# Kernel tuning notes

Hardware: AMD Instinct MI355X
Metric: run time of the kernel (lower is better)

## Reference

```python
import jax, jax.numpy as jnp
import numpy as np

N = 100000   # num_nodes
E = 1600000  # num_edges
R = 8        # num_rels
B = 4        # num_bases
D = 64       # inp_dim = h_dim = out_dim


def setup_inputs() -> dict:
    key = jax.random.key(0)
    ks = jax.random.split(key, 16)
    s = 1.0 / np.sqrt(D)
    inp = {
        'h': jax.random.normal(ks[0], (N, D), jnp.float32),
        'src': jax.random.randint(ks[1], (E,), 0, N),
        'dst': jax.random.randint(ks[2], (E,), 0, N),
        'etype': jax.random.randint(ks[3], (E,), 0, R),
        'norm': jax.random.uniform(ks[4], (E, 1), jnp.float32),
    }
    for i in range(3):  # i2h, hidden, h2o layers (basis decomposition)
        inp[f'bases{i}'] = jax.random.normal(ks[5 + 2 * i], (B, D, D), jnp.float32) * s
        inp[f'wcomp{i}'] = jax.random.normal(ks[6 + 2 * i], (R, B), jnp.float32) * s
    inp['dec_w1'] = jax.random.normal(ks[11], (D, D), jnp.float32) * s
    inp['dec_b1'] = jnp.zeros((D,), jnp.float32)
    inp['dec_w2'] = jax.random.normal(ks[12], (D, 1), jnp.float32) * s
    inp['dec_b2'] = jnp.zeros((1,), jnp.float32)
    return inp


def rgcn_layer(h, src, dst, etype, norm, bases, wcomp, activate):
    # basis decomposition: W_r = sum_b wcomp[r,b] * bases[b]
    W = jnp.einsum('rb,bio->rio', wcomp, bases)           # [R, D, D]
    # transform all nodes under every relation (dense GEMM), then gather per edge
    Ht = jnp.einsum('ni,rio->rno', h, W).reshape(R * N, -1)  # [R*N, D]
    msg = Ht[etype * N + src] * norm                      # [E, D] gather + norm
    out = jax.ops.segment_sum(msg, dst, num_segments=N)   # scatter-add to dst
    return jax.nn.relu(out) if activate else out


def reference(h, src, dst, etype, norm, bases0, wcomp0, bases1, wcomp1,
              bases2, wcomp2, dec_w1, dec_b1, dec_w2, dec_b2):
    # EncoderRGCN: i2h (relu) -> hidden (relu) -> h2o (no activation)
    h1 = rgcn_layer(h, src, dst, etype, norm, bases0, wcomp0, True)
    h2 = rgcn_layer(h1, src, dst, etype, norm, bases1, wcomp1, True)
    henc = rgcn_layer(h2, src, dst, etype, norm, bases2, wcomp2, False)
    # AttributeDecoder: Linear -> ReLU -> Linear(reconstruct_dim=1)
    d1 = jax.nn.relu(henc @ dec_w1 + dec_b1)
    rec = (d1 @ dec_w2 + dec_b2).squeeze()                # [N]
    return rec, henc
```

## Files before the change

### kernel.cpp

```cpp
#include <hip/hip_runtime.h>

typedef _Float16 half8 __attribute__((ext_vector_type(8)));
typedef _Float16 half4 __attribute__((ext_vector_type(4)));
typedef _Float16 half2v __attribute__((ext_vector_type(2)));
typedef float floatx4 __attribute__((ext_vector_type(4)));

constexpr int NN = 100000;
constexpr int EE = 1600000;
constexpr int NBK = 196;
constexpr int CHUNK = 3125;
constexpr int CAPB = 12288;
constexpr int NDCAP = 48;

__global__ __launch_bounds__(256) void k_part(const int* __restrict__ dst,
                                              const int* __restrict__ src,
                                              const int* __restrict__ etype,
                                              const float* __restrict__ norm,
                                              int* __restrict__ gcur,
                                              int2* __restrict__ part) {
  __shared__ int2 ldata[CHUNK];
  __shared__ unsigned char lbkt[CHUNK];
  __shared__ int lhist[NBK], lbase[NBK + 1], lcur[NBK], gbase[NBK];
  __shared__ int sh[256];
  const int tid = threadIdx.x;
  const int e0 = blockIdx.x * CHUNK;

  for (int b = tid; b < NBK; b += 256) lhist[b] = 0;
  __syncthreads();
  for (int i = tid; i < CHUNK; i += 256)
    atomicAdd(&lhist[dst[e0 + i] >> 9], 1);
  __syncthreads();
  {
    const int v = (tid < NBK) ? lhist[tid] : 0;
    sh[tid] = v;
    __syncthreads();
    int run = v;
    for (int d = 1; d < 256; d <<= 1) {
      int t = (tid >= d) ? sh[tid - d] : 0;
      __syncthreads();
      run += t;
      sh[tid] = run;
      __syncthreads();
    }
    if (tid < NBK) {
      lbase[tid] = run - v;
      lcur[tid] = 0;
      gbase[tid] = tid * CAPB + atomicAdd(&gcur[tid], v);
    }
    if (tid == 0) lbase[NBK] = CHUNK;
  }
  __syncthreads();
  for (int i = tid; i < CHUNK; i += 256) {
    const int e = e0 + i;
    const int d = dst[e], s = src[e], et = etype[e];
    const _Float16 nh = (_Float16)norm[e];
    const unsigned short n16 = __builtin_bit_cast(unsigned short, nh);
    const int bk = d >> 9;
    const int pos = lbase[bk] + atomicAdd(&lcur[bk], 1);
    ldata[pos] = make_int2((d << 15) | (s >> 2), (s & 3) | (et << 2) | ((int)n16 << 5));
    lbkt[pos] = (unsigned char)bk;
  }
  __syncthreads();
  for (int i = tid; i < CHUNK; i += 256) {
    const int bk = (int)lbkt[i];
    part[gbase[bk] + (i - lbase[bk])] = ldata[i];
  }
}

__global__ __launch_bounds__(512) void k_part2(const int* __restrict__ gcur,
                                               const int2* __restrict__ part,
                                               int* __restrict__ off,
                                               int2* __restrict__ em) {
  __shared__ int hcnt[512];
  __shared__ int wred[8];
  __shared__ int swsum[8];
  const int tid = threadIdx.x;
  const int bk = blockIdx.x;
  const int nb0 = bk << 9;
  const int2* __restrict__ pp = part + (size_t)bk * CAPB;

  {
    int pv = (tid < bk) ? gcur[tid] : 0;
    for (int d = 32; d > 0; d >>= 1) pv += __shfl_down(pv, d);
    if ((tid & 63) == 0) wred[tid >> 6] = pv;
  }
  hcnt[tid] = 0;
  __syncthreads();
  int base = 0;
#pragma unroll
  for (int w = 0; w < 8; ++w) base += wred[w];
  const int cntb = gcur[bk];

  for (int i = tid; i < cntb; i += 512)
    atomicAdd(&hcnt[(((unsigned)pp[i].x) >> 15) & 511], 1);
  __syncthreads();
  const int v = hcnt[tid];
  int incl = v;
  for (int d = 1; d < 64; d <<= 1) {
    const int t = __shfl_up(incl, d);
    if ((tid & 63) >= d) incl += t;
  }
  if ((tid & 63) == 63) swsum[tid >> 6] = incl;
  __syncthreads();
  int pre = 0;
  for (int w = 0; w < (tid >> 6); ++w) pre += swsum[w];
  const int excl = pre + incl - v;
  {
    const int n = nb0 + tid;
    if (n < NN) off[n] = base + excl;
  }
  if (bk == NBK - 1 && tid == 0) off[NN] = EE;
  hcnt[tid] = excl;
  __syncthreads();
  for (int i = tid; i < cntb; i += 512) {
    const int2 r = pp[i];
    const int d = ((unsigned)r.x) >> 15;
    const int s = ((r.x & 0x7FFF) << 2) | (r.y & 3);
    const int et = (r.y >> 2) & 7;
    const unsigned short n16 = (unsigned short)((r.y >> 5) & 0xFFFF);
    const float nf = (float)__builtin_bit_cast(_Float16, n16);
    const int pos = atomicAdd(&hcnt[d & 511], 1);
    em[base + pos] = make_int2((et << 20) | s, __float_as_int(nf));
  }
}


__global__ __launch_bounds__(256) void k_prep(const float* __restrict__ h,
                                              _Float16* __restrict__ hh,
                                              const float* __restrict__ b0,
                                              const float* __restrict__ b1,
                                              const float* __restrict__ b2,
                                              _Float16* __restrict__ bbt,
                                              int* __restrict__ gcur) {
  const int bx = blockIdx.x;
  if (bx == 0 && threadIdx.x < NBK) gcur[threadIdx.x] = 0;
  if (bx < 6250) {
    const int i = bx * 256 + threadIdx.x;
    const float4 v = *(const float4*)&h[(size_t)i * 4];
    half4 o = {(_Float16)v.x, (_Float16)v.y, (_Float16)v.z, (_Float16)v.w};
    *(half4*)&hh[(size_t)i * 4] = o;
  } else {
    const int g = (bx - 6250) >> 6;
    const int idx = ((bx - 6250) & 63) * 256 + threadIdx.x;
    const float* bases = (g == 0) ? b0 : (g == 1) ? b1 : b2;
    const int o = idx >> 8, k = idx & 255;
    const int b = k >> 6, i = k & 63;
    bbt[g * 16384 + idx] = (_Float16)bases[b * 4096 + i * 64 + o];
  }
}

__global__ __launch_bounds__(256, 8) void k_layer(const _Float16* __restrict__ hh,
                                                  const int* __restrict__ off,
                                                  const int2* __restrict__ em,
                                                  const float* __restrict__ wcomp,
                                                  const _Float16* __restrict__ bbt,
                                                  _Float16* __restrict__ out16,
                                                  float* __restrict__ out32) {
  __shared__ _Float16 Ash[16 * 264];
  __shared__ int  ems_s[16 * NDCAP];
  __shared__ int2 ems_c[16 * NDCAP];
  __shared__ float4 wcs[8];
  __shared__ int offs[17];
  __shared__ int ovf;
  const int tid = threadIdx.x;
  const int lane = tid & 63;
  const int wv = tid >> 6;
  const int n0 = blockIdx.x * 16;

  if (tid < 17) offs[tid] = off[n0 + tid];
  if (tid == 0) ovf = 0;
  if (tid < 8) wcs[tid] = ((const float4*)wcomp)[tid];
  for (int i = tid; i < 16 * NDCAP; i += 256) {
    ems_s[i] = 0;
    ems_c[i] = make_int2(0, 0);
  }
  __syncthreads();

  const int e0 = offs[0];
  const int len = offs[16] - e0;
  for (int i = tid; i < len; i += 256) {
    const int g = e0 + i;
    const int2 r = em[g];
    int lo = 0, hi = 15;
    while (lo < hi) { const int mid = (lo + hi + 1) >> 1; if (offs[mid] <= g) lo = mid; else hi = mid - 1; }
    const int rank = g - offs[lo];
    const int et = r.x >> 20;
    const int s = r.x & 0xFFFFF;
    const float nf = __int_as_float(r.y);
    const float4 w = wcs[et];
    const _Float16 c0 = (_Float16)(nf * w.x), c1 = (_Float16)(nf * w.y);
    const _Float16 c2 = (_Float16)(nf * w.z), c3 = (_Float16)(nf * w.w);
    const half2v p01 = {c0, c1}, p23 = {c2, c3};
    if (rank < NDCAP) {
      ems_s[lo * NDCAP + rank] = s;
      ems_c[lo * NDCAP + rank] = make_int2(
          __builtin_bit_cast(int, p01), __builtin_bit_cast(int, p23));
    } else ovf = 1;
  }
  __syncthreads();

  if (!ovf) {
    const int fl = lane & 31;
    const int eg = lane >> 5;
    const half2v* __restrict__ hp = (const half2v*)hh;
    for (int q = 0; q < 4; ++q) {
      const int m = wv * 4 + q;
      const int cnt = offs[m + 1] - offs[m];
      const int nbat = (cnt + 15) >> 4;
      const int* sp = &ems_s[m * NDCAP + eg * 8];
      const int2* cp = &ems_c[m * NDCAP + eg * 8];
      half2v a0 = {0, 0}, a1 = {0, 0}, a2 = {0, 0}, a3 = {0, 0};
      for (int b = 0; b < nbat; ++b) {
        int s8[8];
#pragma unroll
        for (int j = 0; j < 8; ++j) s8[j] = sp[b * 16 + j];
        half2v hv[8];
#pragma unroll
        for (int j = 0; j < 8; ++j)
          hv[j] = hp[(unsigned)s8[j] * 32u + fl];
#pragma unroll
        for (int j = 0; j < 8; ++j) {
          const int2 cc = cp[b * 16 + j];
          const half2v c01 = __builtin_bit_cast(half2v, cc.x);
          const half2v c23 = __builtin_bit_cast(half2v, cc.y);
          a0 = a0 + hv[j] * __builtin_shufflevector(c01, c01, 0, 0);
          a1 = a1 + hv[j] * __builtin_shufflevector(c01, c01, 1, 1);
          a2 = a2 + hv[j] * __builtin_shufflevector(c23, c23, 0, 0);
          a3 = a3 + hv[j] * __builtin_shufflevector(c23, c23, 1, 1);
        }
      }
      a0 = a0 + __builtin_bit_cast(half2v, __shfl_xor(__builtin_bit_cast(int, a0), 32));
      a1 = a1 + __builtin_bit_cast(half2v, __shfl_xor(__builtin_bit_cast(int, a1), 32));
      a2 = a2 + __builtin_bit_cast(half2v, __shfl_xor(__builtin_bit_cast(int, a2), 32));
      a3 = a3 + __builtin_bit_cast(half2v, __shfl_xor(__builtin_bit_cast(int, a3), 32));
      if (eg == 0) {
        _Float16* ar = &Ash[m * 264];
        *(half2v*)&ar[0 * 64 + 2 * fl] = a0;
        *(half2v*)&ar[1 * 64 + 2 * fl] = a1;
        *(half2v*)&ar[2 * 64 + 2 * fl] = a2;
        *(half2v*)&ar[3 * 64 + 2 * fl] = a3;
      }
    }
  } else {
    const _Float16* hl = hh + lane;
    for (int q = 0; q < 4; ++q) {
      const int m = wv * 4 + q;
      const int p0 = offs[m], p1 = offs[m + 1];
      float a0 = 0.f, a1 = 0.f, a2 = 0.f, a3 = 0.f;
      for (int p = p0; p < p1; p += 8) {
#pragma unroll
        for (int j = 0; j < 8; ++j) {
          const bool live = (p + j < p1);
          const int idx = live ? p + j : p1 - 1;
          const int2 mm = em[idx];
          const float hv = (float)hl[(size_t)(mm.x & 0xFFFFF) << 6];
          const float wn = live ? __int_as_float(mm.y) : 0.f;
          const float4 w = wcs[mm.x >> 20];
          const float t = wn * hv;
          a0 = fmaf(t, w.x, a0); a1 = fmaf(t, w.y, a1);
          a2 = fmaf(t, w.z, a2); a3 = fmaf(t, w.w, a3);
        }
      }
      _Float16* ar = &Ash[m * 264];
      ar[lane]       = (_Float16)a0;
      ar[64 + lane]  = (_Float16)a1;
      ar[128 + lane] = (_Float16)a2;
      ar[192 + lane] = (_Float16)a3;
    }
  }
  __syncthreads();

  const int col = lane & 15;
  const int quad = lane >> 4;
  const int obase = wv * 16 + col;
  const _Float16* ap = &Ash[col * 264 + quad * 8];
  const _Float16* bp = &bbt[(size_t)obase * 256 + quad * 8];
  floatx4 acc = {0.f, 0.f, 0.f, 0.f};
#pragma unroll
  for (int s = 0; s < 8; ++s) {
    const half8 af = *(const half8*)(ap + s * 32);
    const half8 bf = *(const half8*)(bp + s * 32);
    acc = __builtin_amdgcn_mfma_f32_16x16x32_f16(af, bf, acc, 0, 0, 0);
  }
  if (out16) {
#pragma unroll
    for (int r = 0; r < 4; ++r) {
      const float c = fmaxf(acc[r], 0.f);
      out16[(size_t)(n0 + quad * 4 + r) * 64 + obase] = (_Float16)c;
    }
  } else {
#pragma unroll
    for (int r = 0; r < 4; ++r) {
      out32[(size_t)(n0 + quad * 4 + r) * 64 + obase] = acc[r];
    }
  }
}

__global__ __launch_bounds__(256) void k_dec(const float* __restrict__ henc,
                                             const float* __restrict__ w1,
                                             const float* __restrict__ b1,
                                             const float* __restrict__ w2,
                                             const float* __restrict__ b2,
                                             float* __restrict__ rec) {
  __shared__ float w1s[64 * 64];
  __shared__ float hs[16 * 68];
  const int tid = threadIdx.x;
  for (int r = tid; r < 1024; r += 256)
    *(float4*)&w1s[r * 4] = *(const float4*)&w1[r * 4];
  const int og = tid & 15;
  const int nl = tid >> 4;
  const float4 wv2 = *(const float4*)&w2[og * 4];
  const float4 bv1 = *(const float4*)&b1[og * 4];
  const float b2v = b2[0];
  for (int t0 = blockIdx.x * 16; t0 < NN; t0 += gridDim.x * 16) {
    __syncthreads();
    {
      const float4 hv = *(const float4*)&henc[(size_t)t0 * 64 + tid * 4];
      *(float4*)&hs[(tid >> 4) * 68 + (tid & 15) * 4] = hv;
    }
    __syncthreads();
    float4 acc = bv1;
    const float* hr = &hs[nl * 68];
#pragma unroll 8
    for (int i = 0; i < 64; ++i) {
      const float hv = hr[i];
      const float4 wv = *(const float4*)&w1s[i * 64 + og * 4];
      acc.x = fmaf(hv, wv.x, acc.x); acc.y = fmaf(hv, wv.y, acc.y);
      acc.z = fmaf(hv, wv.z, acc.z); acc.w = fmaf(hv, wv.w, acc.w);
    }
    acc.x = fmaxf(acc.x, 0.f); acc.y = fmaxf(acc.y, 0.f);
    acc.z = fmaxf(acc.z, 0.f); acc.w = fmaxf(acc.w, 0.f);
    float v = acc.x * wv2.x + acc.y * wv2.y + acc.z * wv2.z + acc.w * wv2.w;
    v += __shfl_xor(v, 1); v += __shfl_xor(v, 2);
    v += __shfl_xor(v, 4); v += __shfl_xor(v, 8);
    if (og == 0) rec[t0 + nl] = v + b2v;
  }
}


extern "C" void kernel_launch(void* const* d_in, const int* in_sizes, int n_in,
                              void* d_out, int out_size, void* d_ws, size_t ws_size,
                              hipStream_t stream) {
  const float* h     = (const float*)d_in[0];
  const int*   src   = (const int*)d_in[1];
  const int*   dst   = (const int*)d_in[2];
  const int*   etype = (const int*)d_in[3];
  const float* norm  = (const float*)d_in[4];
  const float* bases[3] = {(const float*)d_in[5], (const float*)d_in[7], (const float*)d_in[9]};
  const float* wcomp[3] = {(const float*)d_in[6], (const float*)d_in[8], (const float*)d_in[10]};
  const float* dw1 = (const float*)d_in[11];
  const float* db1 = (const float*)d_in[12];
  const float* dw2 = (const float*)d_in[13];
  const float* db2 = (const float*)d_in[14];

  float* rec  = (float*)d_out;
  float* henc = (float*)d_out + NN;

  char* ws = (char*)d_ws;
  int*      off    = (int*)(ws + 0);
  int*      gcur   = (int*)(ws + 400512);
  int2*     em     = (int2*)(ws + 402560);
  _Float16* hh     = (_Float16*)(ws + 13202560);
  _Float16* h1f    = (_Float16*)(ws + 26002560);
  _Float16* h2f    = (_Float16*)(ws + 38802560);
  _Float16* bbt    = (_Float16*)(ws + 51602560);
  int2*     part   = (int2*)h1f;

  k_prep<<<6250 + 192, 256, 0, stream>>>(h, hh, bases[0], bases[1], bases[2], bbt, gcur);

  k_part<<<512, 256, 0, stream>>>(dst, src, etype, norm, gcur, part);
  k_part2<<<NBK, 512, 0, stream>>>(gcur, part, off, em);

  k_layer<<<NN / 16, 256, 0, stream>>>(hh,  off, em, wcomp[0], bbt,         h1f, nullptr);
  k_layer<<<NN / 16, 256, 0, stream>>>(h1f, off, em, wcomp[1], bbt + 16384, h2f, nullptr);
  k_layer<<<NN / 16, 256, 0, stream>>>(h2f, off, em, wcomp[2], bbt + 32768, nullptr, henc);

  k_dec<<<256, 256, 0, stream>>>(henc, dw1, db1, dw2, db2, rec);
}
```

Baseline: 347.3 us.

## Encode local dst index in edge records and software-pipeline gather across nodes

Packs the destination node's low four bits into the edge record during partitioning, so the layer kernel no longer binary-searches offsets per edge. Restructures the per-wave gather loop to double-buffer the hh row loads, prefetching the next node's first batch while the current node's FMAs run, and uses int4 vector LDS loads for indices and coefficients. Also vectorises the shared-memory zeroing. This adds register pressure from two eight-entry buffers and sixteen accumulators, which could reduce occupancy.

```diff
diff --git a/kernel.cpp b/kernel.cpp
--- a/kernel.cpp
+++ b/kernel.cpp
@@ -120,7 +120,7 @@
     const unsigned short n16 = (unsigned short)((r.y >> 5) & 0xFFFF);
     const float nf = (float)__builtin_bit_cast(_Float16, n16);
     const int pos = atomicAdd(&hcnt[d & 511], 1);
-    em[base + pos] = make_int2((et << 20) | s, __float_as_int(nf));
+    em[base + pos] = make_int2(((d & 15) << 23) | (et << 20) | s, __float_as_int(nf));
   }
 }
 
@@ -170,9 +170,12 @@
   if (tid < 17) offs[tid] = off[n0 + tid];
   if (tid == 0) ovf = 0;
   if (tid < 8) wcs[tid] = ((const float4*)wcomp)[tid];
-  for (int i = tid; i < 16 * NDCAP; i += 256) {
-    ems_s[i] = 0;
-    ems_c[i] = make_int2(0, 0);
+  {
+    const int4 z4 = make_int4(0, 0, 0, 0);
+    int4* zs = (int4*)ems_s;
+    int4* zc = (int4*)ems_c;
+    if (tid < 192) zs[tid] = z4;
+    for (int i = tid; i < 384; i += 256) zc[i] = z4;
   }
   __syncthreads();
 
@@ -181,10 +184,9 @@
   for (int i = tid; i < len; i += 256) {
     const int g = e0 + i;
     const int2 r = em[g];
-    int lo = 0, hi = 15;
-    while (lo < hi) { const int mid = (lo + hi + 1) >> 1; if (offs[mid] <= g) lo = mid; else hi = mid - 1; }
+    const int lo = (r.x >> 23) & 15;
     const int rank = g - offs[lo];
-    const int et = r.x >> 20;
+    const int et = (r.x >> 20) & 7;
     const int s = r.x & 0xFFFFF;
     const float nf = __int_as_float(r.y);
     const float4 w = wcs[et];
@@ -199,46 +201,91 @@
   }
   __syncthreads();
 
+#define LOADB(mm, bb, hv)                                                      \
+  {                                                                            \
+    const int4* sp4_ = (const int4*)&ems_s[(mm) * NDCAP + (bb) * 16 + eg * 8]; \
+    const int4 sa_ = sp4_[0], sb_ = sp4_[1];                                   \
+    hv[0] = hp[(unsigned)sa_.x * 32u + fl];                                    \
+    hv[1] = hp[(unsigned)sa_.y * 32u + fl];                                    \
+    hv[2] = hp[(unsigned)sa_.z * 32u + fl];                                    \
+    hv[3] = hp[(unsigned)sa_.w * 32u + fl];                                    \
+    hv[4] = hp[(unsigned)sb_.x * 32u + fl];                                    \
+    hv[5] = hp[(unsigned)sb_.y * 32u + fl];                                    \
+    hv[6] = hp[(unsigned)sb_.z * 32u + fl];                                    \
+    hv[7] = hp[(unsigned)sb_.w * 32u + fl];                                    \
+  }
+
+#define FMAQ(mm, bb, hv, aq)                                                   \
+  {                                                                            \
+    const int4* cp4_ = (const int4*)&ems_c[(mm) * NDCAP + (bb) * 16 + eg * 8]; \
+    _Pragma("unroll")                                                          \
+    for (int k_ = 0; k_ < 4; ++k_) {                                           \
+      const int4 c_ = cp4_[k_];                                                \
+      const half2v pa01_ = __builtin_bit_cast(half2v, c_.x);                   \
+      const half2v pa23_ = __builtin_bit_cast(half2v, c_.y);                   \
+      const half2v pb01_ = __builtin_bit_cast(half2v, c_.z);                   \
+      const half2v pb23_ = __builtin_bit_cast(half2v, c_.w);                   \
+      aq[0] = aq[0] + hv[2 * k_] * __builtin_shufflevector(pa01_, pa01_, 0, 0);\
+      aq[1] = aq[1] + hv[2 * k_] * __builtin_shufflevector(pa01_, pa01_, 1, 1);\
+      aq[2] = aq[2] + hv[2 * k_] * __builtin_shufflevector(pa23_, pa23_, 0, 0);\
+      aq[3] = aq[3] + hv[2 * k_] * __builtin_shufflevector(pa23_, pa23_, 1, 1);\
+      aq[0] = aq[0] + hv[2 * k_ + 1] * __builtin_shufflevector(pb01_, pb01_, 0, 0);\
+      aq[1] = aq[1] + hv[2 * k_ + 1] * __builtin_shufflevector(pb01_, pb01_, 1, 1);\
+      aq[2] = aq[2] + hv[2 * k_ + 1] * __builtin_shufflevector(pb23_, pb23_, 0, 0);\
+      aq[3] = aq[3] + hv[2 * k_ + 1] * __builtin_shufflevector(pb23_, pb23_, 1, 1);\
+    }                                                                          \
+  }
+
   if (!ovf) {
     const int fl = lane & 31;
     const int eg = lane >> 5;
     const half2v* __restrict__ hp = (const half2v*)hh;
+    const int mb = wv * 4;
+    const int oA = offs[mb], oB = offs[mb + 1], oC = offs[mb + 2],
+              oD = offs[mb + 3], oE = offs[mb + 4];
+    const int c0n = oB - oA, c1n = oC - oB, c2n = oD - oC, c3n = oE - oD;
+    const int nb0_ = (c0n > 0) ? ((c0n + 15) >> 4) : 1;
+    const int nb1_ = (c1n > 0) ? ((c1n + 15) >> 4) : 1;
+    const int nb2_ = (c2n > 0) ? ((c2n + 15) >> 4) : 1;
+    const int nb3_ = (c3n > 0) ? ((c3n + 15) >> 4) : 1;
+
+    half2v acc[4][4];
+#pragma unroll
+    for (int q = 0; q < 4; ++q)
+#pragma unroll
+      for (int i = 0; i < 4; ++i) acc[q][i] = half2v{0, 0};
+
+    half2v hvA[8], hvB[8];
+    LOADB(mb, 0, hvA);
+#pragma unroll
     for (int q = 0; q < 4; ++q) {
-      const int m = wv * 4 + q;
-      const int cnt = offs[m + 1] - offs[m];
-      const int nbat = (cnt + 15) >> 4;
-      const int* sp = &ems_s[m * NDCAP + eg * 8];
-      const int2* cp = &ems_c[m * NDCAP + eg * 8];
-      half2v a0 = {0, 0}, a1 = {0, 0}, a2 = {0, 0}, a3 = {0, 0};
-      for (int b = 0; b < nbat; ++b) {
-        int s8[8];
-#pragma unroll
-        for (int j = 0; j < 8; ++j) s8[j] = sp[b * 16 + j];
-        half2v hv[8];
-#pragma unroll
-        for (int j = 0; j < 8; ++j)
-          hv[j] = hp[(unsigned)s8[j] * 32u + fl];
-#pragma unroll
-        for (int j = 0; j < 8; ++j) {
-          const int2 cc = cp[b * 16 + j];
-          const half2v c01 = __builtin_bit_cast(half2v, cc.x);
-          const half2v c23 = __builtin_bit_cast(half2v, cc.y);
-          a0 = a0 + hv[j] * __builtin_shufflevector(c01, c01, 0, 0);
-          a1 = a1 + hv[j] * __builtin_shufflevector(c01, c01, 1, 1);
-          a2 = a2 + hv[j] * __builtin_shufflevector(c23, c23, 0, 0);
-          a3 = a3 + hv[j] * __builtin_shufflevector(c23, c23, 1, 1);
+      const int m = mb + q;
+      const int nbq = (q == 0) ? nb0_ : (q == 1) ? nb1_ : (q == 2) ? nb2_ : nb3_;
+      if (q < 3) {
+        if (q & 1) LOADB(m + 1, 0, hvA) else LOADB(m + 1, 0, hvB)
+      }
+      if (q & 1) FMAQ(m, 0, hvB, acc[q]) else FMAQ(m, 0, hvA, acc[q])
+      for (int b = 1; b < nbq; ++b) {
+        if (q & 1) {
+          LOADB(m, b, hvB) FMAQ(m, b, hvB, acc[q])
+        } else {
+          LOADB(m, b, hvA) FMAQ(m, b, hvA, acc[q])
         }
       }
-      a0 = a0 + __builtin_bit_cast(half2v, __shfl_xor(__builtin_bit_cast(int, a0), 32));
-      a1 = a1 + __builtin_bit_cast(half2v, __shfl_xor(__builtin_bit_cast(int, a1), 32));
-      a2 = a2 + __builtin_bit_cast(half2v, __shfl_xor(__builtin_bit_cast(int, a2), 32));
-      a3 = a3 + __builtin_bit_cast(half2v, __shfl_xor(__builtin_bit_cast(int, a3), 32));
+    }
+#pragma unroll
+    for (int q = 0; q < 4; ++q) {
+      const int m = mb + q;
+#pragma unroll
+      for (int i = 0; i < 4; ++i)
+        acc[q][i] = acc[q][i] + __builtin_bit_cast(half2v,
+            __shfl_xor(__builtin_bit_cast(int, acc[q][i]), 32));
       if (eg == 0) {
         _Float16* ar = &Ash[m * 264];
-        *(half2v*)&ar[0 * 64 + 2 * fl] = a0;
-        *(half2v*)&ar[1 * 64 + 2 * fl] = a1;
-        *(half2v*)&ar[2 * 64 + 2 * fl] = a2;
-        *(half2v*)&ar[3 * 64 + 2 * fl] = a3;
+        *(half2v*)&ar[0 * 64 + 2 * fl] = acc[q][0];
+        *(half2v*)&ar[1 * 64 + 2 * fl] = acc[q][1];
+        *(half2v*)&ar[2 * 64 + 2 * fl] = acc[q][2];
+        *(half2v*)&ar[3 * 64 + 2 * fl] = acc[q][3];
       }
     }
   } else {
@@ -255,7 +302,7 @@
           const int2 mm = em[idx];
           const float hv = (float)hl[(size_t)(mm.x & 0xFFFFF) << 6];
           const float wn = live ? __int_as_float(mm.y) : 0.f;
-          const float4 w = wcs[mm.x >> 20];
+          const float4 w = wcs[(mm.x >> 20) & 7];
           const float t = wn * hv;
           a0 = fmaf(t, w.x, a0); a1 = fmaf(t, w.y, a1);
           a2 = fmaf(t, w.z, a2); a3 = fmaf(t, w.w, a3);
@@ -275,25 +322,27 @@
   const int obase = wv * 16 + col;
   const _Float16* ap = &Ash[col * 264 + quad * 8];
   const _Float16* bp = &bbt[(size_t)obase * 256 + quad * 8];
-  floatx4 acc = {0.f, 0.f, 0.f, 0.f};
+  floatx4 acc2 = {0.f, 0.f, 0.f, 0.f};
 #pragma unroll
   for (int s = 0; s < 8; ++s) {
     const half8 af = *(const half8*)(ap + s * 32);
     const half8 bf = *(const half8*)(bp + s * 32);
-    acc = __builtin_amdgcn_mfma_f32_16x16x32_f16(af, bf, acc, 0, 0, 0);
+    acc2 = __builtin_amdgcn_mfma_f32_16x16x32_f16(af, bf, acc2, 0, 0, 0);
   }
   if (out16) {
 #pragma unroll
     for (int r = 0; r < 4; ++r) {
-      const float c = fmaxf(acc[r], 0.f);
+      const float c = fmaxf(acc2[r], 0.f);
       out16[(size_t)(n0 + quad * 4 + r) * 64 + obase] = (_Float16)c;
     }
   } else {
 #pragma unroll
     for (int r = 0; r < 4; ++r) {
-      out32[(size_t)(n0 + quad * 4 + r) * 64 + obase] = acc[r];
-    }
-  }
+      out32[(size_t)(n0 + quad * 4 + r) * 64 + obase] = acc2[r];
+    }
+  }
+#undef LOADB
+#undef FMAQ
 }
 
 __global__ __launch_bounds__(256) void k_dec(const float* __restrict__ henc,
```

New measurement: 350.2 us. No clear change (+0.8%).
